# Optimization experiments

Measured on AMD Instinct MI355X. Metric: run time of the kernel, lower is better.

The kernel has to match this reference:

```python
import jax, jax.numpy as jnp
import numpy as np

B, L, D, H = 4, 2048, 256, 8
FF = 128  # ff_intermediary_depth hard-coded in module
EPS = 1e-5


def layer_norm(x, g, b):
    mu = jnp.mean(x, axis=-1, keepdims=True)
    var = jnp.mean(jnp.square(x - mu), axis=-1, keepdims=True)
    return (x - mu) * jax.lax.rsqrt(var + EPS) * g + b


def setup_inputs() -> dict:
    key = jax.random.key(0)
    ks = jax.random.split(key, 8)
    s = 1.0 / np.sqrt(D)
    return {
        "seq": jax.random.normal(ks[0], (B, L, D), dtype=jnp.float32),
        "Wq": jax.random.normal(ks[1], (D, D * H), dtype=jnp.float32) * s,
        "Wk": jax.random.normal(ks[2], (D, D * H), dtype=jnp.float32) * s,
        "Wv": jax.random.normal(ks[3], (D, D * H), dtype=jnp.float32) * s,
        "Wo": jax.random.normal(ks[4], (D * H, D), dtype=jnp.float32) * (1.0 / np.sqrt(D * H)),
        "ln1_g": jnp.ones((D,), jnp.float32),
        "ln1_b": jnp.zeros((D,), jnp.float32),
        "W1": jax.random.normal(ks[5], (D, FF), dtype=jnp.float32) * s,
        "b1": jnp.zeros((FF,), jnp.float32),
        "W2": jax.random.normal(ks[6], (FF, D), dtype=jnp.float32) * (1.0 / np.sqrt(FF)),
        "b2": jnp.zeros((D,), jnp.float32),
        "ln2_g": jnp.ones((D,), jnp.float32),
        "ln2_b": jnp.zeros((D,), jnp.float32),
    }


def reference(seq, Wq, Wk, Wv, Wo, ln1_g, ln1_b, W1, b1, W2, b2, ln2_g, ln2_b):
    b, l, d = seq.shape
    # per-head dim equals full depth d (module quirk)
    q = (seq @ Wq).reshape(b, l, H, d)
    k = (seq @ Wk).reshape(b, l, H, d)
    v = (seq @ Wv).reshape(b, l, H, d)
    scores = jnp.einsum('bqhd,bkhd->bhqk', q, k) / jnp.sqrt(jnp.float32(d))
    a = jax.nn.softmax(scores, axis=-1)
    heads = jnp.einsum('bhqk,bkhd->bqhd', a, v).reshape(b, l, H * d)
    att_out = heads @ Wo
    x = layer_norm(seq + att_out, ln1_g, ln1_b)
    ff = jax.nn.relu(x @ W1 + b1) @ W2 + b2
    return layer_norm(x + ff, ln2_g, ln2_b)
```

## Files before the change

### kernel.cpp

```cpp
#include <hip/hip_runtime.h>


typedef unsigned short u16;
typedef unsigned int   u32;
typedef __bf16 bf16x8 __attribute__((ext_vector_type(8)));
typedef __bf16 bf16x2 __attribute__((ext_vector_type(2)));
typedef float  f32x4  __attribute__((ext_vector_type(4)));

#define MFMA(a, b, c) __builtin_amdgcn_mfma_f32_16x16x32_bf16(a, b, c, 0, 0, 0)

#if __has_builtin(__builtin_amdgcn_exp2f)
#define EXP2(x) __builtin_amdgcn_exp2f(x)
#else
#define EXP2(x) exp2f(x)
#endif

#if __has_builtin(__builtin_amdgcn_permlane16_swap) && \
    __has_builtin(__builtin_amdgcn_permlane32_swap)
#define HAS_PERMSWAP 1
#else
#define HAS_PERMSWAP 0
#endif

#define CEXP 0.09016844f

__device__ __forceinline__ float b2f(u16 h) {
  return __uint_as_float(((u32)h) << 16);
}
__device__ __forceinline__ u16 f2b(float f) {
  u32 u = __float_as_uint(f);
  u += 0x7FFFu + ((u >> 16) & 1u);
  return (u16)(u >> 16);
}
__device__ __forceinline__ u32 pkbf(float lo, float hi) {
  bf16x2 v;
  v[0] = (__bf16)lo;
  v[1] = (__bf16)hi;
  return __builtin_bit_cast(u32, v);
}
__device__ __forceinline__ bf16x8 ldb8(const u16* p) { return *(const bf16x8*)p; }

typedef const __attribute__((address_space(1))) u32* gas1_t;
typedef __attribute__((address_space(3))) u32* las3_t;
__device__ __forceinline__ void gload_lds16(const u16* g, u16* lds_base) {
  __builtin_amdgcn_global_load_lds((gas1_t)(const void*)g,
                                   (las3_t)(void*)lds_base, 16, 0, 0);
}

__device__ __forceinline__ int detect_f32(const void* seq) {
  const u32* s = (const u32*)seq;
  int cnt = 0;
  #pragma unroll
  for (int i = 0; i < 64; i++) {
    u32 e = (s[i] >> 7) & 0xFFu;
    cnt += (e >= 100u && e <= 140u) ? 1 : 0;
  }
  return cnt < 48;
}

__device__ __forceinline__ u16 ldw(const void* W, size_t idx, int isf32) {
  return isf32 ? f2b(((const float*)W)[idx]) : ((const u16*)W)[idx];
}

#if HAS_PERMSWAP
__device__ __forceinline__ bf16x8 softmax_pa(f32x4 sn0, f32x4 sn1,
                                             float& lsum) {
  float p00 = EXP2(sn0[0]), p01 = EXP2(sn0[1]);
  float p02 = EXP2(sn0[2]), p03 = EXP2(sn0[3]);
  float p10 = EXP2(sn1[0]), p11 = EXP2(sn1[1]);
  float p12 = EXP2(sn1[2]), p13 = EXP2(sn1[3]);
  lsum += ((p00 + p01) + (p02 + p03)) + ((p10 + p11) + (p12 + p13));
  u32 A0 = pkbf(p00, p01), A1 = pkbf(p02, p03);
  u32 B0 = pkbf(p10, p11), B1 = pkbf(p12, p13);
  auto ra = __builtin_amdgcn_permlane32_swap(A0, B0, false, false);
  auto rb = __builtin_amdgcn_permlane32_swap(A1, B1, false, false);
  auto sa = __builtin_amdgcn_permlane16_swap(ra[0], ra[1], false, false);
  auto sb = __builtin_amdgcn_permlane16_swap(rb[0], rb[1], false, false);
  uint4 wv;
  wv.x = sa[0];
  wv.y = sb[0];
  wv.z = sa[1];
  wv.w = sb[1];
  return __builtin_bit_cast(bf16x8, wv);
}
#endif

__device__ __forceinline__ void ingest_body(
    int bx, int tid, int isf32,
    const void* __restrict__ seq, const void* __restrict__ g1,
    const void* __restrict__ be1, const void* __restrict__ b1,
    const void* __restrict__ b2v, const void* __restrict__ g2,
    const void* __restrict__ be2, u16* __restrict__ sbuf,
    u16* __restrict__ vecs) {
  if (bx < 2048) {
    size_t i = (size_t)bx * 1024 + tid * 4;
    if (isf32) {
      const float* sp = (const float*)seq;
      u16 o0 = f2b(sp[i]), o1 = f2b(sp[i + 1]), o2 = f2b(sp[i + 2]), o3 = f2b(sp[i + 3]);
      uint2 ov; ov.x = (u32)o0 | ((u32)o1 << 16); ov.y = (u32)o2 | ((u32)o3 << 16);
      *(uint2*)(sbuf + i) = ov;
    } else {
      *(uint2*)(sbuf + i) = ((const uint2*)seq)[i >> 2];
    }
  } else {
    int t = bx - 2048;
    const void* src; int n;
    switch (t) {
      case 0: src = g1;  n = 256; break;
      case 1: src = be1; n = 256; break;
      case 2: src = b1;  n = 128; break;
      case 3: src = b2v; n = 256; break;
      case 4: src = g2;  n = 256; break;
      default: src = be2; n = 256; break;
    }
    if (tid < n) vecs[t * 256 + tid] = ldw(src, tid, isf32);
  }
}

__device__ __forceinline__ void pack_body(
    int px, int py, int tid, int isf32,
    const void* __restrict__ Wq, const void* __restrict__ Wk,
    const void* __restrict__ Wv, const void* __restrict__ Wo,
    const void* __restrict__ W1, const void* __restrict__ W2,
    u16* __restrict__ pWq, u16* __restrict__ pWk, u16* __restrict__ pWv,
    u16* __restrict__ pWo, u16* __restrict__ pW1, u16* __restrict__ pW2) {
  const void* W; u16* P; int K, N;
  switch (py) {
    case 0: W = Wq; P = pWq; K = 256;  N = 2048; break;
    case 1: W = Wk; P = pWk; K = 256;  N = 2048; break;
    case 2: W = Wv; P = pWv; K = 256;  N = 2048; break;
    case 3: W = Wo; P = pWo; K = 2048; N = 256;  break;
    case 4: W = W1; P = pW1; K = 256;  N = 128;  break;
    default: W = W2; P = pW2; K = 128; N = 256;  break;
  }
  int t = px * 256 + tid;
  int total = (K >> 5) * (N >> 4) * 64;
  if (t >= total) return;
  int lane = t & 63, f = t >> 6;
  int NT = N >> 4;
  int kt = f / NT, nt = f - kt * NT;
  int row0 = kt * 32 + ((lane >> 4) << 3);
  int col = nt * 16 + (lane & 15);
  u16 e[8];
  #pragma unroll
  for (int j = 0; j < 8; j++) e[j] = ldw(W, (size_t)(row0 + j) * N + col, isf32);
  uint4 u;
  u.x = (u32)e[0] | ((u32)e[1] << 16);
  u.y = (u32)e[2] | ((u32)e[3] << 16);
  u.z = (u32)e[4] | ((u32)e[5] << 16);
  u.w = (u32)e[6] | ((u32)e[7] << 16);
  *(uint4*)(P + ((size_t)f * 64 + lane) * 8) = u;
}

__global__ __launch_bounds__(256) void ingest_pack_kernel(
    const void* __restrict__ seq, const void* __restrict__ g1,
    const void* __restrict__ be1, const void* __restrict__ b1,
    const void* __restrict__ b2v, const void* __restrict__ g2,
    const void* __restrict__ be2, u16* __restrict__ sbuf,
    u16* __restrict__ vecs,
    const void* __restrict__ Wq, const void* __restrict__ Wk,
    const void* __restrict__ Wv, const void* __restrict__ Wo,
    const void* __restrict__ W1, const void* __restrict__ W2,
    u16* __restrict__ pWq, u16* __restrict__ pWk, u16* __restrict__ pWv,
    u16* __restrict__ pWo, u16* __restrict__ pW1, u16* __restrict__ pW2) {
  int isf32 = detect_f32(seq);
  int bx = blockIdx.x, tid = threadIdx.x;
  if (bx < 2054) {
    ingest_body(bx, tid, isf32, seq, g1, be1, b1, b2v, g2, be2, sbuf, vecs);
  } else {
    int bxp = bx - 2054;
    pack_body(bxp & 255, bxp >> 8, tid, isf32, Wq, Wk, Wv, Wo, W1, W2,
              pWq, pWk, pWv, pWo, pW1, pW2);
  }
}

__global__ __launch_bounds__(256, 2) void qkv_kernel(
    const u16* __restrict__ X,
    const u16* __restrict__ pWq, const u16* __restrict__ pWk,
    const u16* __restrict__ pWv,
    u16* __restrict__ Qo, u16* __restrict__ Ko, u16* __restrict__ Vo,
    int ntbase, int hc) {
  __shared__ u16 blds[64 * 512];
  __shared__ u16 ebuf[4 * 1280];
  const u16* Pw = (blockIdx.z == 0) ? pWq : ((blockIdx.z == 1) ? pWk : pWv);
  u16* Out = (blockIdx.z == 0) ? Qo : ((blockIdx.z == 1) ? Ko : Vo);
  int tid = threadIdx.x, lane = tid & 63, w = tid >> 6;
  int nt0 = ntbase + blockIdx.x * 8;
  int isv = (blockIdx.z == 2);
  float sc = (blockIdx.z == 0) ? CEXP : 1.0f;
  int hl = blockIdx.x >> 1;
  int dd0 = (blockIdx.x & 1) * 128;
  u16* eb = ebuf + (size_t)w * 1280;
  #pragma unroll
  for (int i = 0; i < 16; i++) {
    int fl = w + i * 4;
    int kt = fl >> 3, nt = fl & 7;
    gload_lds16(Pw + ((size_t)(kt * 128 + nt0 + nt) * 64 + lane) * 8,
                blds + (size_t)fl * 512);
  }
  bf16x8 af[2][8];
  {
    int m0 = blockIdx.y * 512 + w * 32;
    #pragma unroll
    for (int kt = 0; kt < 8; kt++) {
      af[0][kt] = ldb8(X + (size_t)(m0 + (lane & 15)) * 256 + kt * 32 + (lane >> 4) * 8);
      af[1][kt] = ldb8(X + (size_t)(m0 + 16 + (lane & 15)) * 256 + kt * 32 + (lane >> 4) * 8);
    }
  }
  asm volatile("s_waitcnt vmcnt(0)" ::: "memory");
  __syncthreads();
  for (int y = 0; y < 4; y++) {
    int m0b = blockIdx.y * 512 + y * 128;
    f32x4 acc[2][8] = {};
    #pragma unroll
    for (int kt = 0; kt < 8; kt++) {
      const u16* bp = blds + (size_t)kt * 8 * 512 + (size_t)lane * 8;
      #pragma unroll
      for (int nt = 0; nt < 8; nt++) {
        bf16x8 b = ldb8(bp + nt * 512);
        acc[0][nt] = MFMA(af[0][kt], b, acc[0][nt]);
        acc[1][nt] = MFMA(af[1][kt], b, acc[1][nt]);
      }
    }
    if (y < 3) {
      int m1 = m0b + 128 + w * 32;
      #pragma unroll
      for (int kt = 0; kt < 8; kt++) {
        af[0][kt] = ldb8(X + (size_t)(m1 + (lane & 15)) * 256 + kt * 32 + (lane >> 4) * 8);
        af[1][kt] = ldb8(X + (size_t)(m1 + 16 + (lane & 15)) * 256 + kt * 32 + (lane >> 4) * 8);
      }
    }
    int bi = m0b >> 11, l0 = m0b & 2047;
    if (!isv) {
      #pragma unroll
      for (int g = 0; g < 4; g++) {
        #pragma unroll
        for (int mt = 0; mt < 2; mt++)
          #pragma unroll
          for (int nt2 = 0; nt2 < 2; nt2++) {
            int nt = g * 2 + nt2;
            #pragma unroll
            for (int r = 0; r < 4; r++)
              eb[(mt * 16 + (lane >> 4) * 4 + r) * 40 + nt2 * 16 + (lane & 15)] =
                  f2b(acc[mt][nt][r] * sc);
          }
        asm volatile("s_waitcnt lgkmcnt(0)" ::: "memory");
        #pragma unroll
        for (int rep = 0; rep < 2; rep++) {
          int ch = lane + rep * 64;
          int row = ch >> 2, c8 = ch & 3;
          uint4 v = *(uint4*)(eb + row * 40 + c8 * 8);
          *(uint4*)(Out + ((size_t)(bi * hc + hl) * 2048 + l0 + w * 32 + row) * 256 +
                    dd0 + g * 32 + c8 * 8) = v;
        }
        asm volatile("s_waitcnt lgkmcnt(0)" ::: "memory");
      }
    } else {
      #pragma unroll
      for (int g = 0; g < 4; g++) {
        #pragma unroll
        for (int mt = 0; mt < 2; mt++)
          #pragma unroll
          for (int nt2 = 0; nt2 < 2; nt2++) {
            int nt = g * 2 + nt2;
            #pragma unroll
            for (int r = 0; r < 4; r++)
              eb[(nt2 * 16 + (lane & 15)) * 40 + mt * 16 + (lane >> 4) * 4 + r] =
                  f2b(acc[mt][nt][r]);
          }
        asm volatile("s_waitcnt lgkmcnt(0)" ::: "memory");
        #pragma unroll
        for (int rep = 0; rep < 2; rep++) {
          int ch = lane + rep * 64;
          int dc = ch >> 2, c8 = ch & 3;
          uint4 v = *(uint4*)(eb + dc * 40 + c8 * 8);
          *(uint4*)(Out + ((size_t)(bi * hc + hl) * 256 + dd0 + g * 32 + dc) * 2048 +
                    l0 + w * 32 + c8 * 8) = v;
        }
        asm volatile("s_waitcnt lgkmcnt(0)" ::: "memory");
      }
    }
  }
}

__global__ __launch_bounds__(512, 4) void attn_kernel(
    const u16* __restrict__ Q, const u16* __restrict__ K,
    const u16* __restrict__ Vt, u16* __restrict__ O, int nbh) {
  __shared__ u16 kbuf[2 * 8192];
  __shared__ u16 vbuf[2 * 8192];
#if !HAS_PERMSWAP
  __shared__ u16 plds[8 * 640];
#endif
  int tid = threadIdx.x, lane = tid & 63, w = tid >> 6;
  int bi2 = blockIdx.x;
  int bh, qt;
  if (nbh >= 8) {
    int G = nbh >> 3;
    bh = (bi2 & 7) * G + (bi2 >> 3) % G;
    qt = bi2 / (8 * G);
  } else {
    bh = bi2 % nbh; qt = bi2 / nbh;
  }
  const u16* Qb  = Q  + (size_t)bh * 2048 * 256;
  const u16* Kb  = K  + (size_t)bh * 2048 * 256;
  const u16* Vtb = Vt + (size_t)bh * 256 * 2048;
  u16* Ob = O + (size_t)bh * 2048 * 256;
  int q0 = qt * 128 + w * 16;
  bf16x8 qf[8];
  #pragma unroll
  for (int kt = 0; kt < 8; kt++)
    qf[kt] = ldb8(Qb + (size_t)(q0 + (lane & 15)) * 256 + kt * 32 + (lane >> 4) * 8);
  f32x4 o[16] = {};
  float lsum = 0.f;
#if !HAS_PERMSWAP
  u16* pl = plds + (size_t)w * 640;
#endif

  #pragma unroll
  for (int j = 0; j < 2; j++) {
    int f = w * 2 + j;
    gload_lds16(Kb + (size_t)((f >> 3) * 16 + (lane & 15)) * 256 +
                    (f & 7) * 32 + (lane >> 4) * 8,
                kbuf + f * 512);
    gload_lds16(Vtb + (size_t)(f * 16 + (lane & 15)) * 2048 + (lane >> 4) * 8,
                vbuf + f * 512);
  }

  for (int t = 0; t < 64; t++) {
    int s0i = t * 32;
    asm volatile("s_waitcnt vmcnt(0)\ns_barrier" ::: "memory");
    if (t < 63) {
      int nb = (t + 1) & 1;
      #pragma unroll
      for (int j = 0; j < 2; j++) {
        int f = w * 2 + j;
        gload_lds16(Kb + (size_t)(s0i + 32 + (f >> 3) * 16 + (lane & 15)) * 256 +
                        (f & 7) * 32 + (lane >> 4) * 8,
                    kbuf + nb * 8192 + f * 512);
        gload_lds16(Vtb + (size_t)(f * 16 + (lane & 15)) * 2048 + s0i + 32 +
                        (lane >> 4) * 8,
                    vbuf + nb * 8192 + f * 512);
      }
    }
    const u16* kb = kbuf + (t & 1) * 8192;
    f32x4 s[2] = {};
    __builtin_amdgcn_s_setprio(1);
    #pragma unroll
    for (int ntk = 0; ntk < 2; ntk++)
      #pragma unroll
      for (int kt = 0; kt < 8; kt++) {
        bf16x8 a = ldb8(kb + (size_t)(ntk * 8 + kt) * 512 + lane * 8);
        s[ntk] = MFMA(a, qf[kt], s[ntk]);
      }
    __builtin_amdgcn_s_setprio(0);
#if HAS_PERMSWAP
    bf16x8 pa = softmax_pa(s[0], s[1], lsum);
#else
    #pragma unroll
    for (int ntk = 0; ntk < 2; ntk++) {
      float p0 = EXP2(s[ntk][0]);
      float p1 = EXP2(s[ntk][1]);
      float p2 = EXP2(s[ntk][2]);
      float p3 = EXP2(s[ntk][3]);
      lsum += (p0 + p1) + (p2 + p3);
      uint2 pk;
      pk.x = pkbf(p0, p1);
      pk.y = pkbf(p2, p3);
      *(uint2*)(pl + (lane & 15) * 40 + 16 * ntk + 4 * (lane >> 4)) = pk;
    }
    asm volatile("s_waitcnt lgkmcnt(0)" ::: "memory");
    bf16x8 pa = ldb8(pl + (lane & 15) * 40 + (lane >> 4) * 8);
    asm volatile("s_waitcnt lgkmcnt(0)" ::: "memory");
#endif
    const u16* vb0 = vbuf + (t & 1) * 8192;
    __builtin_amdgcn_s_setprio(1);
    #pragma unroll
    for (int nt = 0; nt < 16; nt++) {
      bf16x8 vb = ldb8(vb0 + (size_t)nt * 512 + lane * 8);
      o[nt] = MFMA(vb, pa, o[nt]);
    }
    __builtin_amdgcn_s_setprio(0);
  }
  float l = lsum;
  l += __shfl_xor(l, 16);
  l += __shfl_xor(l, 32);
  float linv = 1.0f / l;
  u16* el = kbuf + w * 1152;
  __syncthreads();
  #pragma unroll
  for (int g = 0; g < 4; g++) {
    if (g) asm volatile("s_waitcnt lgkmcnt(0)" ::: "memory");
    #pragma unroll
    for (int t2 = 0; t2 < 4; t2++) {
      int nt = g * 4 + t2;
      uint2 pk;
      pk.x = pkbf(o[nt][0] * linv, o[nt][1] * linv);
      pk.y = pkbf(o[nt][2] * linv, o[nt][3] * linv);
      *(uint2*)(el + (lane & 15) * 72 + t2 * 16 + 4 * (lane >> 4)) = pk;
    }
    asm volatile("s_waitcnt lgkmcnt(0)" ::: "memory");
    #pragma unroll
    for (int rep = 0; rep < 2; rep++) {
      int ch = lane + rep * 64;
      int row = ch >> 3, c8 = ch & 7;
      uint4 v = *(uint4*)(el + row * 72 + c8 * 8);
      *(uint4*)(Ob + (size_t)(q0 + row) * 256 + g * 64 + c8 * 8) = v;
    }
  }
}

__global__ __launch_bounds__(128) void accum_ln1_ffn_ln2_kernel(
    const u16* __restrict__ Oc, const u16* __restrict__ pWo,
    const u16* __restrict__ sbuf, const u16* __restrict__ vecs,
    const u16* __restrict__ pW1, const u16* __restrict__ pW2,
    const void* __restrict__ seq, void* __restrict__ out) {
  __shared__ u16 blds[2 * 32 * 512];
  int tid = threadIdx.x, lane = tid & 63, w = tid >> 6;
  int m0 = blockIdx.x * 32 + w * 16;
  int arow = m0 + (lane & 15);
  int bq = arow >> 11, lrow = arow & 2047;
  f32x4 acc[16] = {};
  #pragma unroll
  for (int i = 0; i < 16; i++) {
    int fl = w + i * 2;
    int ktg = fl >> 4, nt = fl & 15;
    gload_lds16(pWo + ((size_t)(ktg * 16 + nt) * 64 + lane) * 8,
                blds + (size_t)fl * 512);
  }
  asm volatile("s_waitcnt vmcnt(0)" ::: "memory");
  __syncthreads();
  for (int r = 0; r < 32; r++) {
    int k0 = r * 2;
    const u16* cur = blds + (size_t)(r & 1) * 16384;
    bf16x8 aA, aB;
    {
      int ktl = k0, hl = ktl >> 3;
      int d0 = (ktl & 7) * 32 + (lane >> 4) * 8;
      aA = ldb8(Oc + ((size_t)(bq * 8 + hl) * 2048 + lrow) * 256 + d0);
      ktl = k0 + 1; hl = ktl >> 3;
      d0 = (ktl & 7) * 32 + (lane >> 4) * 8;
      aB = ldb8(Oc + ((size_t)(bq * 8 + hl) * 2048 + lrow) * 256 + d0);
    }
    if (r < 31) {
      u16* nxt = blds + (size_t)((r + 1) & 1) * 16384;
      #pragma unroll
      for (int i = 0; i < 16; i++) {
        int fl = w + i * 2;
        int ktg = k0 + 2 + (fl >> 4), nt = fl & 15;
        gload_lds16(pWo + ((size_t)(ktg * 16 + nt) * 64 + lane) * 8,
                    nxt + (size_t)fl * 512);
      }
    }
    #pragma unroll
    for (int kl = 0; kl < 2; kl++) {
      bf16x8 a = kl ? aB : aA;
      const u16* bp = cur + (size_t)kl * 16 * 512 + (size_t)lane * 8;
      #pragma unroll
      for (int nt = 0; nt < 16; nt++) {
        bf16x8 b = ldb8(bp + nt * 512);
        acc[nt] = MFMA(a, b, acc[nt]);
      }
    }
    asm volatile("s_waitcnt vmcnt(0)" ::: "memory");
    __syncthreads();
  }
  int rbase = m0 + (lane >> 4) * 4;
  #pragma unroll
  for (int nt = 0; nt < 16; nt++) {
    int d = nt * 16 + (lane & 15);
    #pragma unroll
    for (int r = 0; r < 4; r++)
      acc[nt][r] += b2f(sbuf[(size_t)(rbase + r) * 256 + d]);
  }
  float mu[4], rs[4];
  #pragma unroll
  for (int r = 0; r < 4; r++) {
    float sm = 0.f;
    #pragma unroll
    for (int nt = 0; nt < 16; nt++) sm += acc[nt][r];
    sm += __shfl_xor(sm, 1); sm += __shfl_xor(sm, 2);
    sm += __shfl_xor(sm, 4); sm += __shfl_xor(sm, 8);
    mu[r] = sm * (1.0f / 256.0f);
    float v = 0.f;
    #pragma unroll
    for (int nt = 0; nt < 16; nt++) { float dd = acc[nt][r] - mu[r]; v += dd * dd; }
    v += __shfl_xor(v, 1); v += __shfl_xor(v, 2);
    v += __shfl_xor(v, 4); v += __shfl_xor(v, 8);
    rs[r] = rsqrtf(v * (1.0f / 256.0f) + 1e-5f);
  }
  u16* xw = blds + (size_t)w * 16 * 264;
  uint2 xp[16];
  #pragma unroll
  for (int nt = 0; nt < 16; nt++) {
    int d = nt * 16 + (lane & 15);
    float gg = b2f(vecs[d]), bb = b2f(vecs[256 + d]);
    u16 e[4];
    #pragma unroll
    for (int r = 0; r < 4; r++) {
      e[r] = f2b((acc[nt][r] - mu[r]) * rs[r] * gg + bb);
      xw[((lane >> 4) * 4 + r) * 264 + d] = e[r];
    }
    xp[nt].x = (u32)e[0] | ((u32)e[1] << 16);
    xp[nt].y = (u32)e[2] | ((u32)e[3] << 16);
  }
  __syncthreads();
  int isf32 = detect_f32(seq);
  u16* hb = blds + 16384 + (size_t)w * 16 * 136;
  f32x4 acc1[8] = {};
  #pragma unroll
  for (int kt = 0; kt < 8; kt++) {
    bf16x8 a = ldb8(xw + (size_t)(lane & 15) * 264 + kt * 32 + (lane >> 4) * 8);
    const u16* bp = pW1 + ((size_t)kt * 8 * 64 + lane) * 8;
    #pragma unroll
    for (int nt = 0; nt < 8; nt++) {
      bf16x8 b = ldb8(bp + nt * 512);
      acc1[nt] = MFMA(a, b, acc1[nt]);
    }
  }
  #pragma unroll
  for (int nt = 0; nt < 8; nt++) {
    int col = nt * 16 + (lane & 15);
    float bb = b2f(vecs[512 + col]);
    #pragma unroll
    for (int r = 0; r < 4; r++) {
      float h = fmaxf(acc1[nt][r] + bb, 0.f);
      hb[((lane >> 4) * 4 + r) * 136 + col] = f2b(h);
    }
  }
  __syncthreads();
  f32x4 acc2[16] = {};
  #pragma unroll
  for (int ks = 0; ks < 4; ks++) {
    bf16x8 a = ldb8(hb + (size_t)(lane & 15) * 136 + ks * 32 + (lane >> 4) * 8);
    const u16* bp = pW2 + ((size_t)ks * 16 * 64 + lane) * 8;
    #pragma unroll
    for (int nt = 0; nt < 16; nt++) {
      bf16x8 b = ldb8(bp + nt * 512);
      acc2[nt] = MFMA(a, b, acc2[nt]);
    }
  }
  #pragma unroll
  for (int nt = 0; nt < 16; nt++) {
    int d = nt * 16 + (lane & 15);
    float bb = b2f(vecs[768 + d]);
    acc2[nt][0] += bb + b2f((u16)(xp[nt].x & 0xFFFF));
    acc2[nt][1] += bb + b2f((u16)(xp[nt].x >> 16));
    acc2[nt][2] += bb + b2f((u16)(xp[nt].y & 0xFFFF));
    acc2[nt][3] += bb + b2f((u16)(xp[nt].y >> 16));
  }
  float mu2[4], rs2[4];
  #pragma unroll
  for (int r = 0; r < 4; r++) {
    float sm = 0.f;
    #pragma unroll
    for (int nt = 0; nt < 16; nt++) sm += acc2[nt][r];
    sm += __shfl_xor(sm, 1); sm += __shfl_xor(sm, 2);
    sm += __shfl_xor(sm, 4); sm += __shfl_xor(sm, 8);
    mu2[r] = sm * (1.0f / 256.0f);
    float v = 0.f;
    #pragma unroll
    for (int nt = 0; nt < 16; nt++) { float dd = acc2[nt][r] - mu2[r]; v += dd * dd; }
    v += __shfl_xor(v, 1); v += __shfl_xor(v, 2);
    v += __shfl_xor(v, 4); v += __shfl_xor(v, 8);
    rs2[r] = rsqrtf(v * (1.0f / 256.0f) + 1e-5f);
  }
  #pragma unroll
  for (int nt = 0; nt < 16; nt++) {
    int d = nt * 16 + (lane & 15);
    float gg = b2f(vecs[1024 + d]), bb = b2f(vecs[1280 + d]);
    #pragma unroll
    for (int r = 0; r < 4; r++) {
      float val = (acc2[nt][r] - mu2[r]) * rs2[r] * gg + bb;
      size_t idx = (size_t)(rbase + r) * 256 + d;
      if (isf32) ((float*)out)[idx] = val;
      else       ((u16*)out)[idx]   = f2b(val);
    }
  }
}

__global__ __launch_bounds__(256) void accum_kernel(
    const u16* __restrict__ Oc, const u16* __restrict__ pWo,
    float* __restrict__ att_out, int kt0, int hc) {
  __shared__ u16 blds[64 * 512];
  int tid = threadIdx.x, lane = tid & 63, w = tid >> 6;
  int m0 = blockIdx.x * 64 + w * 16;
  int arow = m0 + (lane & 15);
  int bq = arow >> 11, lrow = arow & 2047;
  int ktn = hc * 8;
  f32x4 acc[16] = {};
  for (int k0 = 0; k0 < ktn; k0 += 4) {
    __syncthreads();
    #pragma unroll
    for (int i = 0; i < 16; i++) {
      int fl = w + i * 4;
      int ktg = kt0 + k0 + (fl >> 4), nt = fl & 15;
      gload_lds16(pWo + ((size_t)(ktg * 16 + nt) * 64 + lane) * 8,
                  blds + (size_t)fl * 512);
    }
    asm volatile("s_waitcnt vmcnt(0)" ::: "memory");
    __syncthreads();
    #pragma unroll
    for (int kl = 0; kl < 4; kl++) {
      int ktl = k0 + kl;
      int hl = ktl >> 3;
      int d0 = (ktl & 7) * 32 + (lane >> 4) * 8;
      bf16x8 a = ldb8(Oc + ((size_t)(bq * hc + hl) * 2048 + lrow) * 256 + d0);
      const u16* bp = blds + (size_t)kl * 16 * 512 + (size_t)lane * 8;
      #pragma unroll
      for (int nt = 0; nt < 16; nt++) {
        bf16x8 b = ldb8(bp + nt * 512);
        acc[nt] = MFMA(a, b, acc[nt]);
      }
    }
  }
  int rbase = m0 + (lane >> 4) * 4;
  #pragma unroll
  for (int nt = 0; nt < 16; nt++) {
    int d = nt * 16 + (lane & 15);
    #pragma unroll
    for (int r = 0; r < 4; r++)
      att_out[(size_t)(rbase + r) * 256 + d] += acc[nt][r];
  }
}

__global__ __launch_bounds__(256) void ln1_kernel(
    const float* __restrict__ att_out, const u16* __restrict__ sbuf,
    const u16* __restrict__ vecs, u16* __restrict__ xout) {
  int tid = threadIdx.x, lane = tid & 63, w = tid >> 6;
  int row = blockIdx.x * 4 + w;
  const float* ar = att_out + (size_t)row * 256;
  f32x4 a = *(const f32x4*)(ar + lane * 4);
  uint2 sv = *(const uint2*)(sbuf + (size_t)row * 256 + lane * 4);
  float y[4];
  y[0] = a[0] + b2f((u16)(sv.x & 0xFFFF));
  y[1] = a[1] + b2f((u16)(sv.x >> 16));
  y[2] = a[2] + b2f((u16)(sv.y & 0xFFFF));
  y[3] = a[3] + b2f((u16)(sv.y >> 16));
  float sm = y[0] + y[1] + y[2] + y[3];
  sm += __shfl_xor(sm, 1);  sm += __shfl_xor(sm, 2);  sm += __shfl_xor(sm, 4);
  sm += __shfl_xor(sm, 8);  sm += __shfl_xor(sm, 16); sm += __shfl_xor(sm, 32);
  float mu = sm * (1.0f / 256.0f);
  float v = 0.f;
  #pragma unroll
  for (int j = 0; j < 4; j++) { float d = y[j] - mu; v += d * d; }
  v += __shfl_xor(v, 1);  v += __shfl_xor(v, 2);  v += __shfl_xor(v, 4);
  v += __shfl_xor(v, 8);  v += __shfl_xor(v, 16); v += __shfl_xor(v, 32);
  float rs = rsqrtf(v * (1.0f / 256.0f) + 1e-5f);
  u16 o[4];
  #pragma unroll
  for (int j = 0; j < 4; j++) {
    int d = lane * 4 + j;
    o[j] = f2b((y[j] - mu) * rs * b2f(vecs[d]) + b2f(vecs[256 + d]));
  }
  uint2 ov; ov.x = (u32)o[0] | ((u32)o[1] << 16); ov.y = (u32)o[2] | ((u32)o[3] << 16);
  *(uint2*)(xout + (size_t)row * 256 + lane * 4) = ov;
}

__global__ __launch_bounds__(128) void ffn_ln2_kernel(
    const u16* __restrict__ x, const u16* __restrict__ pW1,
    const u16* __restrict__ pW2, const u16* __restrict__ vecs,
    const void* __restrict__ seq, void* __restrict__ out) {
  __shared__ u16 hbuf[2 * 16 * 136];
  int isf32 = detect_f32(seq);
  int tid = threadIdx.x, lane = tid & 63, w = tid >> 6;
  int m0 = blockIdx.x * 32 + w * 16;
  int arow = m0 + (lane & 15);
  u16* hb = hbuf + w * 16 * 136;
  f32x4 acc1[8] = {};
  #pragma unroll
  for (int kt = 0; kt < 8; kt++) {
    bf16x8 a = ldb8(x + (size_t)arow * 256 + kt * 32 + (lane >> 4) * 8);
    const u16* bp = pW1 + ((size_t)kt * 8 * 64 + lane) * 8;
    #pragma unroll
    for (int nt = 0; nt < 8; nt++) {
      bf16x8 b = ldb8(bp + nt * 512);
      acc1[nt] = MFMA(a, b, acc1[nt]);
    }
  }
  #pragma unroll
  for (int nt = 0; nt < 8; nt++) {
    int col = nt * 16 + (lane & 15);
    float bb = b2f(vecs[512 + col]);
    #pragma unroll
    for (int r = 0; r < 4; r++) {
      float h = fmaxf(acc1[nt][r] + bb, 0.f);
      hb[((lane >> 4) * 4 + r) * 136 + col] = f2b(h);
    }
  }
  __syncthreads();
  f32x4 acc2[16] = {};
  #pragma unroll
  for (int ks = 0; ks < 4; ks++) {
    bf16x8 a = ldb8(hb + (lane & 15) * 136 + ks * 32 + (lane >> 4) * 8);
    const u16* bp = pW2 + ((size_t)ks * 16 * 64 + lane) * 8;
    #pragma unroll
    for (int nt = 0; nt < 16; nt++) {
      bf16x8 b = ldb8(bp + nt * 512);
      acc2[nt] = MFMA(a, b, acc2[nt]);
    }
  }
  int rbase = m0 + (lane >> 4) * 4;
  #pragma unroll
  for (int nt = 0; nt < 16; nt++) {
    int d = nt * 16 + (lane & 15);
    float bb = b2f(vecs[768 + d]);
    #pragma unroll
    for (int r = 0; r < 4; r++)
      acc2[nt][r] += bb + b2f(x[(size_t)(rbase + r) * 256 + d]);
  }
  float mu[4], rs[4];
  #pragma unroll
  for (int r = 0; r < 4; r++) {
    float sm = 0.f;
    #pragma unroll
    for (int nt = 0; nt < 16; nt++) sm += acc2[nt][r];
    sm += __shfl_xor(sm, 1); sm += __shfl_xor(sm, 2);
    sm += __shfl_xor(sm, 4); sm += __shfl_xor(sm, 8);
    mu[r] = sm * (1.0f / 256.0f);
    float v = 0.f;
    #pragma unroll
    for (int nt = 0; nt < 16; nt++) { float dd = acc2[nt][r] - mu[r]; v += dd * dd; }
    v += __shfl_xor(v, 1); v += __shfl_xor(v, 2);
    v += __shfl_xor(v, 4); v += __shfl_xor(v, 8);
    rs[r] = rsqrtf(v * (1.0f / 256.0f) + 1e-5f);
  }
  #pragma unroll
  for (int nt = 0; nt < 16; nt++) {
    int d = nt * 16 + (lane & 15);
    float gg = b2f(vecs[1024 + d]), bb = b2f(vecs[1280 + d]);
    #pragma unroll
    for (int r = 0; r < 4; r++) {
      float val = (acc2[nt][r] - mu[r]) * rs[r] * gg + bb;
      size_t idx = (size_t)(rbase + r) * 256 + d;
      if (isf32) ((float*)out)[idx] = val;
      else       ((u16*)out)[idx]   = f2b(val);
    }
  }
}

__global__ __launch_bounds__(256) void sentinel_kernel(void* out, int n,
                                                       const void* seq) {
  int isf32 = detect_f32(seq);
  int i = blockIdx.x * 256 + threadIdx.x;
  if (i < n) {
    if (isf32) ((float*)out)[i] = 777.0f;
    else       ((u16*)out)[i]   = 0x4442;
  }
}

extern "C" void kernel_launch(void* const* d_in, const int* in_sizes, int n_in,
                              void* d_out, int out_size, void* d_ws, size_t ws_size,
                              hipStream_t stream) {
  (void)in_sizes; (void)n_in;
  const void* seq  = d_in[0];
  const void* Wq   = d_in[1];
  const void* Wk   = d_in[2];
  const void* Wv   = d_in[3];
  const void* Wo   = d_in[4];
  const void* g1   = d_in[5];
  const void* be1  = d_in[6];
  const void* W1   = d_in[7];
  const void* b1   = d_in[8];
  const void* W2   = d_in[9];
  const void* b2   = d_in[10];
  const void* g2   = d_in[11];
  const void* be2  = d_in[12];

  size_t o = 0;
  u16* ws = (u16*)d_ws;
  u16* pWq = ws + o; o += 524288;
  u16* pWk = ws + o; o += 524288;
  u16* pWv = ws + o; o += 524288;
  u16* pWo = ws + o; o += 524288;
  u16* pW1 = ws + o; o += 32768;
  u16* pW2 = ws + o; o += 32768;
  float* att = (float*)(ws + o); o += 4194304;
  u16* xb   = ws + o; o += 2097152;
  u16* sbuf = ws + o; o += 2097152;
  u16* vecs = ws + o; o += 2048;
  size_t fixed_elems = o;

  int hc = 0;
  for (int c = 8; c >= 1; c >>= 1) {
    size_t need = (fixed_elems + (size_t)4 * c * 2097152) * 2;
    if (need <= ws_size) { hc = c; break; }
  }
  if (hc == 0) {
    sentinel_kernel<<<dim3((out_size + 255) / 256), 256, 0, stream>>>(
        d_out, out_size, seq);
    return;
  }
  u16* Qc = ws + o; o += (size_t)hc * 2097152;
  u16* Kc = ws + o; o += (size_t)hc * 2097152;
  u16* Vc = ws + o; o += (size_t)hc * 2097152;
  u16* Oc = ws + o;

  ingest_pack_kernel<<<dim3(2054 + 1536), 256, 0, stream>>>(
      seq, g1, be1, b1, b2, g2, be2, sbuf, vecs,
      Wq, Wk, Wv, Wo, W1, W2, pWq, pWk, pWv, pWo, pW1, pW2);
  if (hc == 8) {
    qkv_kernel<<<dim3(16, 16, 3), 256, 0, stream>>>(
        sbuf, pWq, pWk, pWv, Qc, Kc, Vc, 0, 8);
    attn_kernel<<<dim3(32 * 16), 512, 0, stream>>>(Qc, Kc, Vc, Oc, 32);
    accum_ln1_ffn_ln2_kernel<<<dim3(256), 128, 0, stream>>>(
        Oc, pWo, sbuf, vecs, pW1, pW2, seq, (void*)d_out);
  } else {
    hipMemsetAsync(att, 0, 2097152 * sizeof(float), stream);
    int nchunks = 8 / hc;
    for (int c = 0; c < nchunks; c++) {
      int nbh = 4 * hc;
      qkv_kernel<<<dim3(2 * hc, 16, 3), 256, 0, stream>>>(
          sbuf, pWq, pWk, pWv, Qc, Kc, Vc, c * hc * 16, hc);
      attn_kernel<<<dim3(nbh * 16), 512, 0, stream>>>(Qc, Kc, Vc, Oc, nbh);
      accum_kernel<<<dim3(128), 256, 0, stream>>>(Oc, pWo, att, c * hc * 8, hc);
    }
    ln1_kernel<<<dim3(2048), 256, 0, stream>>>(att, sbuf, vecs, xb);
    ffn_ln2_kernel<<<dim3(256), 128, 0, stream>>>(xb, pW1, pW2, vecs, seq,
                                                  (void*)d_out);
  }
}
```

Before: 333.8 us.

## Split Wo projection K across two wave pairs, drop LDS staging of Wo

The fused output-projection + LN1 + FFN + LN2 kernel now runs 4 waves per block instead of 2. Each row group's K=2048 reduction over Wo is split in half across two waves, and the partial sums are combined through LDS. Wo tiles are read directly from global memory (L2) rather than double-buffered into LDS with block barriers, and the later barriers are replaced with per-wave LDS waitcnts. The aim is more parallelism in the serial accumulation phase and less barrier overhead, at the cost of one extra LDS reduction and half the waves going idle afterwards.

```diff
diff --git a/kernel.cpp b/kernel.cpp
--- a/kernel.cpp
+++ b/kernel.cpp
@@ -409,61 +409,40 @@
   }
 }
 
-__global__ __launch_bounds__(128) void accum_ln1_ffn_ln2_kernel(
+__global__ __launch_bounds__(256) void accum_ln1_ffn_ln2_kernel(
     const u16* __restrict__ Oc, const u16* __restrict__ pWo,
     const u16* __restrict__ sbuf, const u16* __restrict__ vecs,
     const u16* __restrict__ pW1, const u16* __restrict__ pW2,
     const void* __restrict__ seq, void* __restrict__ out) {
-  __shared__ u16 blds[2 * 32 * 512];
+  __shared__ u16 blds[29184];
   int tid = threadIdx.x, lane = tid & 63, w = tid >> 6;
-  int m0 = blockIdx.x * 32 + w * 16;
+  int rg = w & 1, kh = w >> 1;
+  int m0 = blockIdx.x * 32 + rg * 16;
   int arow = m0 + (lane & 15);
   int bq = arow >> 11, lrow = arow & 2047;
   f32x4 acc[16] = {};
-  #pragma unroll
-  for (int i = 0; i < 16; i++) {
-    int fl = w + i * 2;
-    int ktg = fl >> 4, nt = fl & 15;
-    gload_lds16(pWo + ((size_t)(ktg * 16 + nt) * 64 + lane) * 8,
-                blds + (size_t)fl * 512);
-  }
-  asm volatile("s_waitcnt vmcnt(0)" ::: "memory");
+  int kbase = kh * 32;
+  for (int kt2 = 0; kt2 < 32; kt2++) {
+    int ktl = kbase + kt2;
+    int hl = ktl >> 3;
+    int d0 = (ktl & 7) * 32 + (lane >> 4) * 8;
+    bf16x8 a = ldb8(Oc + ((size_t)(bq * 8 + hl) * 2048 + lrow) * 256 + d0);
+    const u16* bp = pWo + ((size_t)ktl * 16 * 64 + lane) * 8;
+    #pragma unroll
+    for (int nt = 0; nt < 16; nt++) {
+      bf16x8 b = ldb8(bp + nt * 512);
+      acc[nt] = MFMA(a, b, acc[nt]);
+    }
+  }
+  float* rp = (float*)(blds + 12800) + ((size_t)rg * 64 + lane) * 64;
+  if (kh) {
+    #pragma unroll
+    for (int nt = 0; nt < 16; nt++) *(f32x4*)(rp + nt * 4) = acc[nt];
+  }
   __syncthreads();
-  for (int r = 0; r < 32; r++) {
-    int k0 = r * 2;
-    const u16* cur = blds + (size_t)(r & 1) * 16384;
-    bf16x8 aA, aB;
-    {
-      int ktl = k0, hl = ktl >> 3;
-      int d0 = (ktl & 7) * 32 + (lane >> 4) * 8;
-      aA = ldb8(Oc + ((size_t)(bq * 8 + hl) * 2048 + lrow) * 256 + d0);
-      ktl = k0 + 1; hl = ktl >> 3;
-      d0 = (ktl & 7) * 32 + (lane >> 4) * 8;
-      aB = ldb8(Oc + ((size_t)(bq * 8 + hl) * 2048 + lrow) * 256 + d0);
-    }
-    if (r < 31) {
-      u16* nxt = blds + (size_t)((r + 1) & 1) * 16384;
-      #pragma unroll
-      for (int i = 0; i < 16; i++) {
-        int fl = w + i * 2;
-        int ktg = k0 + 2 + (fl >> 4), nt = fl & 15;
-        gload_lds16(pWo + ((size_t)(ktg * 16 + nt) * 64 + lane) * 8,
-                    nxt + (size_t)fl * 512);
-      }
-    }
-    #pragma unroll
-    for (int kl = 0; kl < 2; kl++) {
-      bf16x8 a = kl ? aB : aA;
-      const u16* bp = cur + (size_t)kl * 16 * 512 + (size_t)lane * 8;
-      #pragma unroll
-      for (int nt = 0; nt < 16; nt++) {
-        bf16x8 b = ldb8(bp + nt * 512);
-        acc[nt] = MFMA(a, b, acc[nt]);
-      }
-    }
-    asm volatile("s_waitcnt vmcnt(0)" ::: "memory");
-    __syncthreads();
-  }
+  if (kh) return;
+  #pragma unroll
+  for (int nt = 0; nt < 16; nt++) acc[nt] += *(const f32x4*)(rp + nt * 4);
   int rbase = m0 + (lane >> 4) * 4;
   #pragma unroll
   for (int nt = 0; nt < 16; nt++) {
@@ -488,7 +467,7 @@
     v += __shfl_xor(v, 4); v += __shfl_xor(v, 8);
     rs[r] = rsqrtf(v * (1.0f / 256.0f) + 1e-5f);
   }
-  u16* xw = blds + (size_t)w * 16 * 264;
+  u16* xw = blds + (size_t)rg * 16 * 264;
   uint2 xp[16];
   #pragma unroll
   for (int nt = 0; nt < 16; nt++) {
@@ -503,9 +482,9 @@
     xp[nt].x = (u32)e[0] | ((u32)e[1] << 16);
     xp[nt].y = (u32)e[2] | ((u32)e[3] << 16);
   }
-  __syncthreads();
+  asm volatile("s_waitcnt lgkmcnt(0)" ::: "memory");
   int isf32 = detect_f32(seq);
-  u16* hb = blds + 16384 + (size_t)w * 16 * 136;
+  u16* hb = blds + 8448 + (size_t)rg * 16 * 136;
   f32x4 acc1[8] = {};
   #pragma unroll
   for (int kt = 0; kt < 8; kt++) {
@@ -527,7 +506,7 @@
       hb[((lane >> 4) * 4 + r) * 136 + col] = f2b(h);
     }
   }
-  __syncthreads();
+  asm volatile("s_waitcnt lgkmcnt(0)" ::: "memory");
   f32x4 acc2[16] = {};
   #pragma unroll
   for (int ks = 0; ks < 4; ks++) {
@@ -802,7 +781,7 @@
     qkv_kernel<<<dim3(16, 16, 3), 256, 0, stream>>>(
         sbuf, pWq, pWk, pWv, Qc, Kc, Vc, 0, 8);
     attn_kernel<<<dim3(32 * 16), 512, 0, stream>>>(Qc, Kc, Vc, Oc, 32);
-    accum_ln1_ffn_ln2_kernel<<<dim3(256), 128, 0, stream>>>(
+    accum_ln1_ffn_ln2_kernel<<<dim3(256), 256, 0, stream>>>(
         Oc, pWo, sbuf, vecs, pW1, pW2, seq, (void*)d_out);
   } else {
     hipMemsetAsync(att, 0, 2097152 * sizeof(float), stream);
```

After: 375.0 us. 12.4% more time.
